# Performance work log

Measured on AMD Instinct MI355X. Metric: run time of the kernel, lower is better.

## Reference

```python
import jax, jax.numpy as jnp
import numpy as np

N = 50000   # nodes
E = 800000  # edges (avg degree 16)
D = 64      # isize == hidden_dim
L = 3       # num_gc_layers
BN_EPS = 1e-5


def setup_inputs() -> dict:
    key = jax.random.key(0)
    ks = jax.random.split(key, 8)
    x = jax.random.normal(ks[0], (N, D), dtype=jnp.float32)
    edge_index = jax.random.randint(ks[1], (2, E), 0, N, dtype=jnp.int64)
    # Stacked per-layer MLP params (layer 0 has isize==hidden_dim so shapes match)
    scale = 0.05
    W1 = jax.random.normal(ks[2], (L, D, D), dtype=jnp.float32) * scale
    b1 = jax.random.normal(ks[3], (L, D), dtype=jnp.float32) * scale
    W2 = jax.random.normal(ks[4], (L, D, D), dtype=jnp.float32) * scale
    b2 = jax.random.normal(ks[5], (L, D), dtype=jnp.float32) * scale
    gamma = jnp.ones((L, D), dtype=jnp.float32)
    beta = jnp.zeros((L, D), dtype=jnp.float32)
    return {"x": x, "edge_index": edge_index, "W1": W1, "b1": b1,
            "W2": W2, "b2": b2, "gamma": gamma, "beta": beta}


def reference(x, edge_index, W1, b1, W2, b2, gamma, beta):
    # GINConv (eps=0): h_i' = MLP(x_i + sum_{j->i} x_j), then BatchNorm1d
    # (training-mode batch statistics), ReLU on all but the last layer.
    # Dropout is identity (deterministic / eval).
    src = edge_index[0]
    dst = edge_index[1]
    h = x
    for i in range(L):
        agg = jax.ops.segment_sum(h[src], dst, num_segments=N)  # [N, D] scatter-add
        z = h + agg                                             # (1+eps)*x + agg, eps=0
        z = jnp.maximum(z @ W1[i] + b1[i], 0.0)                 # MLP hidden + ReLU
        z = z @ W2[i] + b2[i]                                   # MLP out
        mean = jnp.mean(z, axis=0)
        var = jnp.var(z, axis=0)                                # biased var, as torch BN
        z = (z - mean) * jax.lax.rsqrt(var + BN_EPS) * gamma[i] + beta[i]
        if i < L - 1:
            z = jnp.maximum(z, 0.0)
        h = z
    return h
```

## Files before the change

kernel.cpp:

```cpp
#include <hip/hip_runtime.h>

#define NN 50000
#define NPAD 50064
#define EE 800000
#define DD 64
#define BN_EPS 1e-5f

#define NPART 8
#define PART_NODES 6250
#define CAP 64
#define BCAP 131072
#define NSCAT 32
#define NB_BUCKET 782
#define NB_AGG  12500
#define NB_MLP  782
#define NB_SETUP 1563
#define NB_APPLY 3125

typedef __attribute__((ext_vector_type(8))) short short8v;
typedef __attribute__((ext_vector_type(4))) float float4v;

__device__ __forceinline__ unsigned bfpack2(float a, float b) {
    union { float f; unsigned u; } ua, ub;
    ua.f = a; ub.f = b;
    unsigned ra = ua.u + 0x7fffu + ((ua.u >> 16) & 1u);
    unsigned rb = ub.u + 0x7fffu + ((ub.u >> 16) & 1u);
    return (ra >> 16) | (rb & 0xffff0000u);
}

__device__ __forceinline__ unsigned short bf16of(float v) {
    union { float f; unsigned u; } x; x.f = v;
    unsigned r = x.u + 0x7fffu + ((x.u >> 16) & 1u);
    return (unsigned short)(r >> 16);
}

__global__ __launch_bounds__(256) void k_setup(const float* __restrict__ x,
                                               unsigned* __restrict__ xb,
                                               const float* __restrict__ W1,
                                               const float* __restrict__ W2,
                                               unsigned short* __restrict__ Wb,
                                               int* __restrict__ bucketCnt,
                                               float* __restrict__ stats) {
    int t = blockIdx.x * 256 + threadIdx.x;
    if (t < NN * 8) {
        const float4* p = (const float4*)(x + (size_t)t * 8);
        float4 a = p[0], b = p[1];
        uint4 o;
        o.x = bfpack2(a.x, a.y); o.y = bfpack2(a.z, a.w);
        o.z = bfpack2(b.x, b.y); o.w = bfpack2(b.z, b.w);
        ((uint4*)xb)[t] = o;
    }
    if (t < 3 * 2 * 4096) {
        int l = t / 8192;
        int rem = t - l * 8192;
        int m = rem / 4096;
        int e = rem - m * 4096;
        int c = e >> 6, k = e & 63;
        const float* W = (m == 0 ? W1 : W2) + l * 4096;
        Wb[t] = bf16of(W[k * 64 + c]);
    }
    if (t < 128) bucketCnt[t] = 0;
    else if (t < 512) stats[t - 128] = 0.f;
}

__global__ __launch_bounds__(1024) void k_build(const int* __restrict__ src,
                                                const int* __restrict__ dst,
                                                unsigned long long* __restrict__ bucket,
                                                int* __restrict__ bucketCnt,
                                                int* __restrict__ cursor) {
    __shared__ int lcnt[8];
    __shared__ int lbase[8];
    int t = threadIdx.x;
    int g = blockIdx.x * 1024 + t;
    if (g < NN) cursor[g] = 0;
    if (t < 8) lcnt[t] = 0;
    __syncthreads();
    int d = 0, s = 0, p = 0, loc = 0;
    bool ok = (g < EE);
    if (ok) {
        d = __builtin_nontemporal_load(dst + g);
        s = __builtin_nontemporal_load(src + g);
        p = (unsigned)d / PART_NODES;
        loc = atomicAdd(&lcnt[p], 1);
    }
    __syncthreads();
    if (t < 8) lbase[t] = atomicAdd(&bucketCnt[t * 16], lcnt[t]);
    __syncthreads();
    if (ok) {
        unsigned long long v = ((unsigned long long)(unsigned)s << 32) | (unsigned)d;
        bucket[(size_t)p * BCAP + lbase[p] + loc] = v;
    }
}

__global__ __launch_bounds__(256) void k_scatter(const unsigned long long* __restrict__ bucket,
                                                 const int* __restrict__ bucketCnt,
                                                 int* __restrict__ cursor,
                                                 int* __restrict__ col) {
    int p = blockIdx.x & 7;
    int cnt = bucketCnt[p * 16];
    const unsigned long long* b = bucket + (size_t)p * BCAP;
    for (int i = (blockIdx.x >> 3) * 256 + threadIdx.x; i < cnt; i += NSCAT * 256) {
        unsigned long long v = __builtin_nontemporal_load(b + i);
        int d = (int)(v & 0xffffffffu);
        int s = (int)(v >> 32);
        int pos = atomicAdd(&cursor[d], 1);
        col[d * CAP + pos] = s;
    }
}

template<int FUSE>
__global__ __launch_bounds__(256) void k_agg4(const unsigned* __restrict__ hb,
                                              const int* __restrict__ deg,
                                              const int* __restrict__ col,
                                              const float* __restrict__ statsL,
                                              const float* __restrict__ gammaL,
                                              const float* __restrict__ betaL,
                                              unsigned* __restrict__ outZb) {
    __shared__ float sa[64];
    __shared__ float sc[64];
    if (FUSE) {
        int tt = threadIdx.x;
        if (tt < 64) {
            float mean = statsL[tt] * (1.f / NN);
            float var = statsL[64 + tt] * (1.f / NN) - mean * mean;
            float a = gammaL[tt] * rsqrtf(var + BN_EPS);
            sa[tt] = a;
            sc[tt] = fmaf(-mean, a, betaL[tt]);
        }
        __syncthreads();
    }
    int node = blockIdx.x * 4 + (threadIdx.x >> 6);
    int lane = threadIdx.x & 63;
    int li = lane & 7;
    int slot = lane >> 3;
    int dn = deg[node];
    int base = node * CAP;
    const uint4* hb4 = (const uint4*)hb;
    float a8[8], c8[8];
    if (FUSE) {
#pragma unroll
        for (int j = 0; j < 8; ++j) { a8[j] = sa[li * 8 + j]; c8[j] = sc[li * 8 + j]; }
    }
    float acc[8];
#pragma unroll
    for (int i = 0; i < 8; ++i) acc[i] = 0.f;

#define UNPK_ADD(U)                                                      \
    {                                                                    \
        uint4 _u = (U);                                                  \
        union { unsigned u; float f; } l0, h0, l1, h1, l2, h2, l3, h3;   \
        l0.u = _u.x << 16; h0.u = _u.x & 0xffff0000u;                    \
        l1.u = _u.y << 16; h1.u = _u.y & 0xffff0000u;                    \
        l2.u = _u.z << 16; h2.u = _u.z & 0xffff0000u;                    \
        l3.u = _u.w << 16; h3.u = _u.w & 0xffff0000u;                    \
        float v[8] = {l0.f, h0.f, l1.f, h1.f, l2.f, h2.f, l3.f, h3.f};   \
        _Pragma("unroll")                                                \
        for (int j = 0; j < 8; ++j)                                      \
            acc[j] += FUSE ? fmaxf(fmaf(v[j], a8[j], c8[j]), 0.f) : v[j];\
    }

    if (slot == 0)
        UNPK_ADD(hb4[(size_t)node * 8 + li]);

    int k = slot;
    for (; k + 8 < dn; k += 16) {
        int s0 = __builtin_nontemporal_load(col + base + k);
        int s1 = __builtin_nontemporal_load(col + base + k + 8);
        uint4 u0 = hb4[(size_t)s0 * 8 + li];
        uint4 u1 = hb4[(size_t)s1 * 8 + li];
        UNPK_ADD(u0);
        UNPK_ADD(u1);
    }
    if (k < dn) {
        int s0 = __builtin_nontemporal_load(col + base + k);
        UNPK_ADD(hb4[(size_t)s0 * 8 + li]);
    }
#undef UNPK_ADD

#pragma unroll
    for (int i = 0; i < 8; ++i) acc[i] += __shfl_xor(acc[i], 8);
#pragma unroll
    for (int i = 0; i < 8; ++i) acc[i] += __shfl_xor(acc[i], 16);
#pragma unroll
    for (int i = 0; i < 8; ++i) acc[i] += __shfl_xor(acc[i], 32);

    if (slot == 0) {
        uint4 o;
        o.x = bfpack2(acc[0], acc[1]);
        o.y = bfpack2(acc[2], acc[3]);
        o.z = bfpack2(acc[4], acc[5]);
        o.w = bfpack2(acc[6], acc[7]);
        ((uint4*)outZb)[(size_t)node * 8 + li] = o;
    }
}

template<int OUTF32>
__global__ __launch_bounds__(256) void k_mlp_mfma(const unsigned short* __restrict__ Zb,
                                                  const unsigned short* __restrict__ WbL,
                                                  const float* __restrict__ b1,
                                                  const float* __restrict__ b2,
                                                  unsigned short* __restrict__ Mb,
                                                  float* __restrict__ Zf,
                                                  float* __restrict__ statsL) {
    __shared__ unsigned short sm[4][16 * 72];
    __shared__ float sred[2][4][64];
    int w = threadIdx.x >> 6;
    int lane = threadIdx.x & 63;
    int q = lane >> 4;
    int cl = lane & 15;
    int r0 = blockIdx.x * 64 + w * 16;

    short8v B1[4][2], B2[4][2];
#pragma unroll
    for (int t = 0; t < 4; ++t) {
#pragma unroll
        for (int h = 0; h < 2; ++h) {
            B1[t][h] = *(const short8v*)(WbL + ((t * 16 + cl) * 64 + h * 32 + q * 8));
            B2[t][h] = *(const short8v*)(WbL + 4096 + ((t * 16 + cl) * 64 + h * 32 + q * 8));
        }
    }

    const unsigned short* zr = Zb + (size_t)(r0 + cl) * 64;
    short8v a0 = *(const short8v*)(zr + q * 8);
    short8v a1 = *(const short8v*)(zr + 32 + q * 8);

    float4v acc1[4];
#pragma unroll
    for (int t = 0; t < 4; ++t) {
        float b = b1[t * 16 + cl];
        acc1[t] = (float4v){b, b, b, b};
        acc1[t] = __builtin_amdgcn_mfma_f32_16x16x32_bf16(a0, B1[t][0], acc1[t], 0, 0, 0);
        acc1[t] = __builtin_amdgcn_mfma_f32_16x16x32_bf16(a1, B1[t][1], acc1[t], 0, 0, 0);
    }

    unsigned short* s = sm[w];
#pragma unroll
    for (int t = 0; t < 4; ++t) {
#pragma unroll
        for (int r = 0; r < 4; ++r) {
            float v = fmaxf(acc1[t][r], 0.f);
            s[(q * 4 + r) * 72 + t * 16 + cl] = bf16of(v);
        }
    }

    short8v a2_0 = *(const short8v*)(s + cl * 72 + q * 8);
    short8v a2_1 = *(const short8v*)(s + cl * 72 + 32 + q * 8);

    float4v acc2[4];
#pragma unroll
    for (int t = 0; t < 4; ++t) {
        float b = b2[t * 16 + cl];
        acc2[t] = (float4v){b, b, b, b};
        acc2[t] = __builtin_amdgcn_mfma_f32_16x16x32_bf16(a2_0, B2[t][0], acc2[t], 0, 0, 0);
        acc2[t] = __builtin_amdgcn_mfma_f32_16x16x32_bf16(a2_1, B2[t][1], acc2[t], 0, 0, 0);
    }

    if (OUTF32) {
#pragma unroll
        for (int t = 0; t < 4; ++t) {
#pragma unroll
            for (int r = 0; r < 4; ++r) {
                int row = r0 + q * 4 + r;
                if (row < NN) Zf[(size_t)row * 64 + t * 16 + cl] = acc2[t][r];
            }
        }
    } else {
#pragma unroll
        for (int t = 0; t < 4; ++t) {
#pragma unroll
            for (int r = 0; r < 4; ++r) {
                s[(q * 4 + r) * 72 + t * 16 + cl] = bf16of(acc2[t][r]);
            }
        }
        short8v m0 = *(const short8v*)(s + cl * 72 + q * 8);
        short8v m1 = *(const short8v*)(s + cl * 72 + 32 + q * 8);
        int orow = r0 + cl;
        if (orow < NN) {
            *(short8v*)(Mb + (size_t)orow * 64 + q * 8) = m0;
            *(short8v*)(Mb + (size_t)orow * 64 + 32 + q * 8) = m1;
        }
    }

#pragma unroll
    for (int t = 0; t < 4; ++t) {
        float sv = 0.f, qv = 0.f;
#pragma unroll
        for (int r = 0; r < 4; ++r) {
            int row = r0 + q * 4 + r;
            float v = (row < NN) ? acc2[t][r] : 0.f;
            sv += v;
            qv = fmaf(v, v, qv);
        }
        sv += __shfl_xor(sv, 16); sv += __shfl_xor(sv, 32);
        qv += __shfl_xor(qv, 16); qv += __shfl_xor(qv, 32);
        if (lane < 16) {
            sred[0][w][t * 16 + cl] = sv;
            sred[1][w][t * 16 + cl] = qv;
        }
    }
    __syncthreads();
    int tt = threadIdx.x;
    if (tt < 128) {
        int which = tt >> 6, c = tt & 63;
        float tot = sred[which][0][c] + sred[which][1][c] +
                    sred[which][2][c] + sred[which][3][c];
        atomicAdd(&statsL[which * 64 + c], tot);
    }
}

__global__ __launch_bounds__(256) void k_apply_aff(const float* __restrict__ B,
                                                   const float* __restrict__ statsL,
                                                   const float* __restrict__ gammaL,
                                                   const float* __restrict__ betaL,
                                                   float* __restrict__ out) {
    __shared__ float sa[64];
    __shared__ float sc[64];
    int t = threadIdx.x;
    if (t < 64) {
        float mean = statsL[t] * (1.f / NN);
        float var = statsL[64 + t] * (1.f / NN) - mean * mean;
        float a = gammaL[t] * rsqrtf(var + BN_EPS);
        sa[t] = a;
        sc[t] = fmaf(-mean, a, betaL[t]);
    }
    __syncthreads();
    int i4 = blockIdx.x * 256 + t;
    if (i4 >= NN * 16) return;
    int cb = (i4 & 15) * 4;
    float4 v = ((const float4*)B)[i4];
    float4 o;
    o.x = fmaf(v.x, sa[cb + 0], sc[cb + 0]);
    o.y = fmaf(v.y, sa[cb + 1], sc[cb + 1]);
    o.z = fmaf(v.z, sa[cb + 2], sc[cb + 2]);
    o.w = fmaf(v.w, sa[cb + 3], sc[cb + 3]);
    ((float4*)out)[i4] = o;
}

extern "C" void kernel_launch(void* const* d_in, const int* in_sizes, int n_in,
                              void* d_out, int out_size, void* d_ws, size_t ws_size,
                              hipStream_t stream) {
    const float* x     = (const float*)d_in[0];
    const int*   ei    = (const int*)d_in[1];
    const float* W1    = (const float*)d_in[2];
    const float* b1    = (const float*)d_in[3];
    const float* W2    = (const float*)d_in[4];
    const float* b2    = (const float*)d_in[5];
    const float* gamma = (const float*)d_in[6];
    const float* beta  = (const float*)d_in[7];
    float* out = (float*)d_out;

    const int* src = ei;
    const int* dst = ei + EE;

    char* w = (char*)d_ws;
    unsigned*       Ab  = (unsigned*)w;       w += (size_t)NPAD * DD * 2;
    unsigned*       Mb  = (unsigned*)w;       w += (size_t)NPAD * DD * 2;
    unsigned*       Xb  = (unsigned*)w;       w += (size_t)NPAD * DD * 2;
    float*          Zf  = (float*)w;          w += (size_t)NN * DD * 4;
    int*            col = (int*)w;            w += (size_t)NN * CAP * 4;
    unsigned long long* bucket = (unsigned long long*)w;
    w += (size_t)NPART * BCAP * 8;
    int*            cursor    = (int*)w;      w += (size_t)NN * 4;
    int*            bucketCnt = (int*)w;      w += 128 * 4;
    float*          stats     = (float*)w;    w += 384 * 4;
    unsigned short* Wb        = (unsigned short*)w; w += 3 * 2 * 4096 * 2;

    k_setup<<<NB_SETUP, 256, 0, stream>>>(x, Xb, W1, W2, Wb, bucketCnt, stats);
    k_build<<<NB_BUCKET, 1024, 0, stream>>>(src, dst, bucket, bucketCnt, cursor);
    k_scatter<<<NPART * NSCAT, 256, 0, stream>>>(bucket, bucketCnt, cursor, col);

    k_agg4<0><<<NB_AGG, 256, 0, stream>>>(Xb, cursor, col, nullptr, nullptr, nullptr, Ab);
    k_mlp_mfma<0><<<NB_MLP, 256, 0, stream>>>((unsigned short*)Ab, Wb, b1, b2,
                                              (unsigned short*)Mb, nullptr, stats);

    k_agg4<1><<<NB_AGG, 256, 0, stream>>>(Mb, cursor, col, stats, gamma, beta, Ab);
    k_mlp_mfma<0><<<NB_MLP, 256, 0, stream>>>((unsigned short*)Ab, Wb + 8192, b1 + 64, b2 + 64,
                                              (unsigned short*)Mb, nullptr, stats + 128);

    k_agg4<1><<<NB_AGG, 256, 0, stream>>>(Mb, cursor, col, stats + 128, gamma + 64, beta + 64, Ab);
    k_mlp_mfma<1><<<NB_MLP, 256, 0, stream>>>((unsigned short*)Ab, Wb + 16384, b1 + 128, b2 + 128,
                                              nullptr, Zf, stats + 256);
    k_apply_aff<<<NB_APPLY, 256, 0, stream>>>(Zf, stats + 256, gamma + 128, beta + 128, out);
}
```

Before: 234.9 us.

## Fuse BatchNorm into MLP via grid barrier and compact edge buckets

The MLP kernel now accumulates the BatchNorm statistics, waits at a software grid-wide barrier (an atomic counter plus a spin-wait), and then applies the normalization and ReLU before writing bf16 output. This removes the fp32 intermediate buffer, the separate apply kernel and the per-edge BN work in the aggregation kernels. Setup work (bf16 conversion of x and the weights) is folded into the bucket-build kernel, and edge buckets are packed into 32-bit words instead of 64-bit. The spin barrier relies on all 782 blocks being resident at once (launch_bounds 256,4), so it can deadlock if occupancy is lower than assumed.

New measurement: 397.4 us. 69.2% more time.

```diff
diff --git a/kernel.cpp b/kernel.cpp
--- a/kernel.cpp
+++ b/kernel.cpp
@@ -11,11 +11,9 @@
 #define CAP 64
 #define BCAP 131072
 #define NSCAT 32
-#define NB_BUCKET 782
+#define NB_BUILD 782
 #define NB_AGG  12500
 #define NB_MLP  782
-#define NB_SETUP 1563
-#define NB_APPLY 3125
 
 typedef __attribute__((ext_vector_type(8))) short short8v;
 typedef __attribute__((ext_vector_type(4))) float float4v;
@@ -34,101 +32,85 @@
     return (unsigned short)(r >> 16);
 }
 
-__global__ __launch_bounds__(256) void k_setup(const float* __restrict__ x,
-                                               unsigned* __restrict__ xb,
-                                               const float* __restrict__ W1,
-                                               const float* __restrict__ W2,
-                                               unsigned short* __restrict__ Wb,
-                                               int* __restrict__ bucketCnt,
-                                               float* __restrict__ stats) {
-    int t = blockIdx.x * 256 + threadIdx.x;
-    if (t < NN * 8) {
-        const float4* p = (const float4*)(x + (size_t)t * 8);
-        float4 a = p[0], b = p[1];
-        uint4 o;
-        o.x = bfpack2(a.x, a.y); o.y = bfpack2(a.z, a.w);
-        o.z = bfpack2(b.x, b.y); o.w = bfpack2(b.z, b.w);
-        ((uint4*)xb)[t] = o;
-    }
-    if (t < 3 * 2 * 4096) {
-        int l = t / 8192;
-        int rem = t - l * 8192;
-        int m = rem / 4096;
-        int e = rem - m * 4096;
-        int c = e >> 6, k = e & 63;
-        const float* W = (m == 0 ? W1 : W2) + l * 4096;
-        Wb[t] = bf16of(W[k * 64 + c]);
-    }
+__global__ void k_zero(int* __restrict__ bucketCnt, float* __restrict__ stats) {
+    int t = threadIdx.x;
     if (t < 128) bucketCnt[t] = 0;
-    else if (t < 512) stats[t - 128] = 0.f;
+    if (t < 384) stats[t] = 0.f;
 }
 
 __global__ __launch_bounds__(1024) void k_build(const int* __restrict__ src,
                                                 const int* __restrict__ dst,
-                                                unsigned long long* __restrict__ bucket,
+                                                unsigned* __restrict__ bucket,
                                                 int* __restrict__ bucketCnt,
-                                                int* __restrict__ cursor) {
+                                                int* __restrict__ cursor,
+                                                const float* __restrict__ x,
+                                                unsigned* __restrict__ xb,
+                                                const float* __restrict__ W1,
+                                                const float* __restrict__ W2,
+                                                unsigned short* __restrict__ Wb) {
     __shared__ int lcnt[8];
     __shared__ int lbase[8];
     int t = threadIdx.x;
     int g = blockIdx.x * 1024 + t;
     if (g < NN) cursor[g] = 0;
+    if (g < NN * 8) {
+        const float4* p = (const float4*)(x + (size_t)g * 8);
+        float4 a = p[0], b = p[1];
+        uint4 o;
+        o.x = bfpack2(a.x, a.y); o.y = bfpack2(a.z, a.w);
+        o.z = bfpack2(b.x, b.y); o.w = bfpack2(b.z, b.w);
+        ((uint4*)xb)[g] = o;
+    }
+    if (g < 3 * 2 * 4096) {
+        int l = g / 8192;
+        int rem = g - l * 8192;
+        int m = rem / 4096;
+        int e = rem - m * 4096;
+        int c = e >> 6, k = e & 63;
+        const float* W = (m == 0 ? W1 : W2) + l * 4096;
+        Wb[g] = bf16of(W[k * 64 + c]);
+    }
     if (t < 8) lcnt[t] = 0;
     __syncthreads();
-    int d = 0, s = 0, p = 0, loc = 0;
+    int p = 0, loc = 0;
+    unsigned pk = 0;
     bool ok = (g < EE);
     if (ok) {
-        d = __builtin_nontemporal_load(dst + g);
-        s = __builtin_nontemporal_load(src + g);
+        int d = __builtin_nontemporal_load(dst + g);
+        int s = __builtin_nontemporal_load(src + g);
         p = (unsigned)d / PART_NODES;
+        pk = ((unsigned)s << 13) | (unsigned)(d - p * PART_NODES);
         loc = atomicAdd(&lcnt[p], 1);
     }
     __syncthreads();
     if (t < 8) lbase[t] = atomicAdd(&bucketCnt[t * 16], lcnt[t]);
     __syncthreads();
-    if (ok) {
-        unsigned long long v = ((unsigned long long)(unsigned)s << 32) | (unsigned)d;
-        bucket[(size_t)p * BCAP + lbase[p] + loc] = v;
-    }
-}
-
-__global__ __launch_bounds__(256) void k_scatter(const unsigned long long* __restrict__ bucket,
+    if (ok) bucket[(size_t)p * BCAP + lbase[p] + loc] = pk;
+}
+
+__global__ __launch_bounds__(256) void k_scatter(const unsigned* __restrict__ bucket,
                                                  const int* __restrict__ bucketCnt,
                                                  int* __restrict__ cursor,
                                                  int* __restrict__ col) {
     int p = blockIdx.x & 7;
     int cnt = bucketCnt[p * 16];
-    const unsigned long long* b = bucket + (size_t)p * BCAP;
+    int dbase = p * PART_NODES;
+    const unsigned* b = bucket + (size_t)p * BCAP;
     for (int i = (blockIdx.x >> 3) * 256 + threadIdx.x; i < cnt; i += NSCAT * 256) {
-        unsigned long long v = __builtin_nontemporal_load(b + i);
-        int d = (int)(v & 0xffffffffu);
-        int s = (int)(v >> 32);
+        unsigned v = __builtin_nontemporal_load(b + i);
+        int d = dbase + (int)(v & 8191u);
+        int s = (int)(v >> 13);
         int pos = atomicAdd(&cursor[d], 1);
         col[d * CAP + pos] = s;
     }
 }
 
-template<int FUSE>
 __global__ __launch_bounds__(256) void k_agg4(const unsigned* __restrict__ hb,
                                               const int* __restrict__ deg,
                                               const int* __restrict__ col,
-                                              const float* __restrict__ statsL,
-                                              const float* __restrict__ gammaL,
-                                              const float* __restrict__ betaL,
+                                              int* __restrict__ bcnt,
                                               unsigned* __restrict__ outZb) {
-    __shared__ float sa[64];
-    __shared__ float sc[64];
-    if (FUSE) {
-        int tt = threadIdx.x;
-        if (tt < 64) {
-            float mean = statsL[tt] * (1.f / NN);
-            float var = statsL[64 + tt] * (1.f / NN) - mean * mean;
-            float a = gammaL[tt] * rsqrtf(var + BN_EPS);
-            sa[tt] = a;
-            sc[tt] = fmaf(-mean, a, betaL[tt]);
-        }
-        __syncthreads();
-    }
+    if (blockIdx.x == 0 && threadIdx.x == 0) *bcnt = 0;
     int node = blockIdx.x * 4 + (threadIdx.x >> 6);
     int lane = threadIdx.x & 63;
     int li = lane & 7;
@@ -136,11 +118,6 @@
     int dn = deg[node];
     int base = node * CAP;
     const uint4* hb4 = (const uint4*)hb;
-    float a8[8], c8[8];
-    if (FUSE) {
-#pragma unroll
-        for (int j = 0; j < 8; ++j) { a8[j] = sa[li * 8 + j]; c8[j] = sc[li * 8 + j]; }
-    }
     float acc[8];
 #pragma unroll
     for (int i = 0; i < 8; ++i) acc[i] = 0.f;
@@ -153,10 +130,8 @@
         l1.u = _u.y << 16; h1.u = _u.y & 0xffff0000u;                    \
         l2.u = _u.z << 16; h2.u = _u.z & 0xffff0000u;                    \
         l3.u = _u.w << 16; h3.u = _u.w & 0xffff0000u;                    \
-        float v[8] = {l0.f, h0.f, l1.f, h1.f, l2.f, h2.f, l3.f, h3.f};   \
-        _Pragma("unroll")                                                \
-        for (int j = 0; j < 8; ++j)                                      \
-            acc[j] += FUSE ? fmaxf(fmaf(v[j], a8[j], c8[j]), 0.f) : v[j];\
+        acc[0] += l0.f; acc[1] += h0.f; acc[2] += l1.f; acc[3] += h1.f;  \
+        acc[4] += l2.f; acc[5] += h2.f; acc[6] += l3.f; acc[7] += h3.f;  \
     }
 
     if (slot == 0)
@@ -194,30 +169,33 @@
     }
 }
 
-template<int OUTF32>
-__global__ __launch_bounds__(256) void k_mlp_mfma(const unsigned short* __restrict__ Zb,
+template<int FINAL>
+__global__ __launch_bounds__(256, 4) void k_mlpbn(const unsigned short* __restrict__ Zb,
                                                   const unsigned short* __restrict__ WbL,
                                                   const float* __restrict__ b1,
                                                   const float* __restrict__ b2,
+                                                  const float* __restrict__ gammaL,
+                                                  const float* __restrict__ betaL,
+                                                  float* __restrict__ statsL,
+                                                  int* __restrict__ bcnt,
                                                   unsigned short* __restrict__ Mb,
-                                                  float* __restrict__ Zf,
-                                                  float* __restrict__ statsL) {
+                                                  float* __restrict__ outF) {
     __shared__ unsigned short sm[4][16 * 72];
     __shared__ float sred[2][4][64];
+    __shared__ float sa[64];
+    __shared__ float sc[64];
     int w = threadIdx.x >> 6;
     int lane = threadIdx.x & 63;
     int q = lane >> 4;
     int cl = lane & 15;
     int r0 = blockIdx.x * 64 + w * 16;
 
-    short8v B1[4][2], B2[4][2];
-#pragma unroll
-    for (int t = 0; t < 4; ++t) {
-#pragma unroll
-        for (int h = 0; h < 2; ++h) {
+    short8v B1[4][2];
+#pragma unroll
+    for (int t = 0; t < 4; ++t) {
+#pragma unroll
+        for (int h = 0; h < 2; ++h)
             B1[t][h] = *(const short8v*)(WbL + ((t * 16 + cl) * 64 + h * 32 + q * 8));
-            B2[t][h] = *(const short8v*)(WbL + 4096 + ((t * 16 + cl) * 64 + h * 32 + q * 8));
-        }
     }
 
     const unsigned short* zr = Zb + (size_t)(r0 + cl) * 64;
@@ -246,6 +224,14 @@
     short8v a2_0 = *(const short8v*)(s + cl * 72 + q * 8);
     short8v a2_1 = *(const short8v*)(s + cl * 72 + 32 + q * 8);
 
+    short8v B2[4][2];
+#pragma unroll
+    for (int t = 0; t < 4; ++t) {
+#pragma unroll
+        for (int h = 0; h < 2; ++h)
+            B2[t][h] = *(const short8v*)(WbL + 4096 + ((t * 16 + cl) * 64 + h * 32 + q * 8));
+    }
+
     float4v acc2[4];
 #pragma unroll
     for (int t = 0; t < 4; ++t) {
@@ -255,23 +241,71 @@
         acc2[t] = __builtin_amdgcn_mfma_f32_16x16x32_bf16(a2_1, B2[t][1], acc2[t], 0, 0, 0);
     }
 
-    if (OUTF32) {
+#pragma unroll
+    for (int t = 0; t < 4; ++t) {
+        float sv = 0.f, qv = 0.f;
+#pragma unroll
+        for (int r = 0; r < 4; ++r) {
+            int row = r0 + q * 4 + r;
+            float v = (row < NN) ? acc2[t][r] : 0.f;
+            sv += v;
+            qv = fmaf(v, v, qv);
+        }
+        sv += __shfl_xor(sv, 16); sv += __shfl_xor(sv, 32);
+        qv += __shfl_xor(qv, 16); qv += __shfl_xor(qv, 32);
+        if (lane < 16) {
+            sred[0][w][t * 16 + cl] = sv;
+            sred[1][w][t * 16 + cl] = qv;
+        }
+    }
+    __syncthreads();
+    int tt = threadIdx.x;
+    if (tt < 128) {
+        int which = tt >> 6, c = tt & 63;
+        float tot = sred[which][0][c] + sred[which][1][c] +
+                    sred[which][2][c] + sred[which][3][c];
+        atomicAdd(&statsL[which * 64 + c], tot);
+    }
+
+    __syncthreads();
+    if (tt == 0) {
+        __threadfence();
+        atomicAdd(bcnt, 1);
+        while (__hip_atomic_load(bcnt, __ATOMIC_ACQUIRE, __HIP_MEMORY_SCOPE_AGENT) < NB_MLP) {}
+    }
+    __syncthreads();
+
+    if (tt < 64) {
+        float mean = statsL[tt] * (1.f / NN);
+        float var = statsL[64 + tt] * (1.f / NN) - mean * mean;
+        float a = gammaL[tt] * rsqrtf(var + BN_EPS);
+        sa[tt] = a;
+        sc[tt] = fmaf(-mean, a, betaL[tt]);
+    }
+    __syncthreads();
+
+    if (FINAL) {
 #pragma unroll
         for (int t = 0; t < 4; ++t) {
+            float a = sa[t * 16 + cl], c = sc[t * 16 + cl];
 #pragma unroll
             for (int r = 0; r < 4; ++r) {
                 int row = r0 + q * 4 + r;
-                if (row < NN) Zf[(size_t)row * 64 + t * 16 + cl] = acc2[t][r];
+                if (row < NN)
+                    outF[(size_t)row * 64 + t * 16 + cl] = fmaf(acc2[t][r], a, c);
             }
         }
     } else {
 #pragma unroll
         for (int t = 0; t < 4; ++t) {
+            float a = sa[t * 16 + cl], c = sc[t * 16 + cl];
 #pragma unroll
             for (int r = 0; r < 4; ++r) {
-                s[(q * 4 + r) * 72 + t * 16 + cl] = bf16of(acc2[t][r]);
+                float y = fmaxf(fmaf(acc2[t][r], a, c), 0.f);
+                s[(q * 4 + r) * 72 + t * 16 + cl] = bf16of(y);
             }
         }
+        __syncthreads();
         short8v m0 = *(const short8v*)(s + cl * 72 + q * 8);
         short8v m1 = *(const short8v*)(s + cl * 72 + 32 + q * 8);
         int orow = r0 + cl;
@@ -280,60 +314,6 @@
             *(short8v*)(Mb + (size_t)orow * 64 + 32 + q * 8) = m1;
         }
     }
-
-#pragma unroll
-    for (int t = 0; t < 4; ++t) {
-        float sv = 0.f, qv = 0.f;
-#pragma unroll
-        for (int r = 0; r < 4; ++r) {
-            int row = r0 + q * 4 + r;
-            float v = (row < NN) ? acc2[t][r] : 0.f;
-            sv += v;
-            qv = fmaf(v, v, qv);
-        }
-        sv += __shfl_xor(sv, 16); sv += __shfl_xor(sv, 32);
-        qv += __shfl_xor(qv, 16); qv += __shfl_xor(qv, 32);
-        if (lane < 16) {
-            sred[0][w][t * 16 + cl] = sv;
-            sred[1][w][t * 16 + cl] = qv;
-        }
-    }
-    __syncthreads();
-    int tt = threadIdx.x;
-    if (tt < 128) {
-        int which = tt >> 6, c = tt & 63;
-        float tot = sred[which][0][c] + sred[which][1][c] +
-                    sred[which][2][c] + sred[which][3][c];
-        atomicAdd(&statsL[which * 64 + c], tot);
-    }
-}
-
-__global__ __launch_bounds__(256) void k_apply_aff(const float* __restrict__ B,
-                                                   const float* __restrict__ statsL,
-                                                   const float* __restrict__ gammaL,
-                                                   const float* __restrict__ betaL,
-                                                   float* __restrict__ out) {
-    __shared__ float sa[64];
-    __shared__ float sc[64];
-    int t = threadIdx.x;
-    if (t < 64) {
-        float mean = statsL[t] * (1.f / NN);
-        float var = statsL[64 + t] * (1.f / NN) - mean * mean;
-        float a = gammaL[t] * rsqrtf(var + BN_EPS);
-        sa[t] = a;
-        sc[t] = fmaf(-mean, a, betaL[t]);
-    }
-    __syncthreads();
-    int i4 = blockIdx.x * 256 + t;
-    if (i4 >= NN * 16) return;
-    int cb = (i4 & 15) * 4;
-    float4 v = ((const float4*)B)[i4];
-    float4 o;
-    o.x = fmaf(v.x, sa[cb + 0], sc[cb + 0]);
-    o.y = fmaf(v.y, sa[cb + 1], sc[cb + 1]);
-    o.z = fmaf(v.z, sa[cb + 2], sc[cb + 2]);
-    o.w = fmaf(v.w, sa[cb + 3], sc[cb + 3]);
-    ((float4*)out)[i4] = o;
 }
 
 extern "C" void kernel_launch(void* const* d_in, const int* in_sizes, int n_in,
@@ -356,29 +336,31 @@
     unsigned*       Ab  = (unsigned*)w;       w += (size_t)NPAD * DD * 2;
     unsigned*       Mb  = (unsigned*)w;       w += (size_t)NPAD * DD * 2;
     unsigned*       Xb  = (unsigned*)w;       w += (size_t)NPAD * DD * 2;
-    float*          Zf  = (float*)w;          w += (size_t)NN * DD * 4;
     int*            col = (int*)w;            w += (size_t)NN * CAP * 4;
-    unsigned long long* bucket = (unsigned long long*)w;
-    w += (size_t)NPART * BCAP * 8;
+    unsigned*       bucket = (unsigned*)w;    w += (size_t)NPART * BCAP * 4;
     int*            cursor    = (int*)w;      w += (size_t)NN * 4;
     int*            bucketCnt = (int*)w;      w += 128 * 4;
     float*          stats     = (float*)w;    w += 384 * 4;
+    int*            bcnt      = (int*)w;      w += 16 * 4;
     unsigned short* Wb        = (unsigned short*)w; w += 3 * 2 * 4096 * 2;
 
-    k_setup<<<NB_SETUP, 256, 0, stream>>>(x, Xb, W1, W2, Wb, bucketCnt, stats);
-    k_build<<<NB_BUCKET, 1024, 0, stream>>>(src, dst, bucket, bucketCnt, cursor);
+    k_zero<<<1, 512, 0, stream>>>(bucketCnt, stats);
+    k_build<<<NB_BUILD, 1024, 0, stream>>>(src, dst, bucket, bucketCnt, cursor,
+                                           x, Xb, W1, W2, Wb);
     k_scatter<<<NPART * NSCAT, 256, 0, stream>>>(bucket, bucketCnt, cursor, col);
 
-    k_agg4<0><<<NB_AGG, 256, 0, stream>>>(Xb, cursor, col, nullptr, nullptr, nullptr, Ab);
-    k_mlp_mfma<0><<<NB_MLP, 256, 0, stream>>>((unsigned short*)Ab, Wb, b1, b2,
-                                              (unsigned short*)Mb, nullptr, stats);
-
-    k_agg4<1><<<NB_AGG, 256, 0, stream>>>(Mb, cursor, col, stats, gamma, beta, Ab);
-    k_mlp_mfma<0><<<NB_MLP, 256, 0, stream>>>((unsigned short*)Ab, Wb + 8192, b1 + 64, b2 + 64,
-                                              (unsigned short*)Mb, nullptr, stats + 128);
-
-    k_agg4<1><<<NB_AGG, 256, 0, stream>>>(Mb, cursor, col, stats + 128, gamma + 64, beta + 64, Ab);
-    k_mlp_mfma<1><<<NB_MLP, 256, 0, stream>>>((unsigned short*)Ab, Wb + 16384, b1 + 128, b2 + 128,
-                                              nullptr, Zf, stats + 256);
-    k_apply_aff<<<NB_APPLY, 256, 0, stream>>>(Zf, stats + 256, gamma + 128, beta + 128, out);
-}
+    k_agg4<<<NB_AGG, 256, 0, stream>>>(Xb, cursor, col, bcnt, Ab);
+    k_mlpbn<0><<<NB_MLP, 256, 0, stream>>>((unsigned short*)Ab, Wb, b1, b2,
+                                           gamma, beta, stats, bcnt,
+                                           (unsigned short*)Mb, nullptr);
+
+    k_agg4<<<NB_AGG, 256, 0, stream>>>(Mb, cursor, col, bcnt + 4, Ab);
+    k_mlpbn<0><<<NB_MLP, 256, 0, stream>>>((unsigned short*)Ab, Wb + 8192, b1 + 64, b2 + 64,
+                                           gamma + 64, beta + 64, stats + 128, bcnt + 4,
+                                           (unsigned short*)Mb, nullptr);
+
+    k_agg4<<<NB_AGG, 256, 0, stream>>>(Mb, cursor, col, bcnt + 8, Ab);
+    k_mlpbn<1><<<NB_MLP, 256, 0, stream>>>((unsigned short*)Ab, Wb + 16384, b1 + 128, b2 + 128,
+                                           gamma + 128, beta + 128, stats + 256, bcnt + 8,
+                                           nullptr, out);
+}
```

## Fuse setup into bucket build, pack bucket entries to 32 bits, widen agg lanes

Applied to the files above, without the earlier changes.

The x and weight bf16 conversion moves into the edge bucketing kernel, and only a tiny zeroing kernel stays separate, so one launch carries both jobs. Bucket entries shrink from 64-bit to 32-bit by storing the source plus a 13-bit destination offset within its partition, halving bucket write and read traffic. The aggregation kernel now uses 4 lanes per row with two uint4 loads each, letting 16 edges be gathered in parallel per node with one edge per slot per iteration. The trade-offs are more registers per lane and a longer shuffle reduction.

Result: slower. 280.3 us (+19.3%).

```diff
diff --git a/kernel.cpp b/kernel.cpp
--- a/kernel.cpp
+++ b/kernel.cpp
@@ -11,10 +11,9 @@
 #define CAP 64
 #define BCAP 131072
 #define NSCAT 32
-#define NB_BUCKET 782
+#define NB_BUILD 782
 #define NB_AGG  12500
 #define NB_MLP  782
-#define NB_SETUP 1563
 #define NB_APPLY 3125
 
 typedef __attribute__((ext_vector_type(8))) short short8v;
@@ -34,82 +33,81 @@
     return (unsigned short)(r >> 16);
 }
 
-__global__ __launch_bounds__(256) void k_setup(const float* __restrict__ x,
-                                               unsigned* __restrict__ xb,
-                                               const float* __restrict__ W1,
-                                               const float* __restrict__ W2,
-                                               unsigned short* __restrict__ Wb,
-                                               int* __restrict__ bucketCnt,
-                                               float* __restrict__ stats) {
-    int t = blockIdx.x * 256 + threadIdx.x;
-    if (t < NN * 8) {
-        const float4* p = (const float4*)(x + (size_t)t * 8);
-        float4 a = p[0], b = p[1];
-        uint4 o;
-        o.x = bfpack2(a.x, a.y); o.y = bfpack2(a.z, a.w);
-        o.z = bfpack2(b.x, b.y); o.w = bfpack2(b.z, b.w);
-        ((uint4*)xb)[t] = o;
-    }
-    if (t < 3 * 2 * 4096) {
-        int l = t / 8192;
-        int rem = t - l * 8192;
-        int m = rem / 4096;
-        int e = rem - m * 4096;
-        int c = e >> 6, k = e & 63;
-        const float* W = (m == 0 ? W1 : W2) + l * 4096;
-        Wb[t] = bf16of(W[k * 64 + c]);
-    }
+__global__ void k_zero(int* __restrict__ bucketCnt, float* __restrict__ stats) {
+    int t = threadIdx.x;
     if (t < 128) bucketCnt[t] = 0;
-    else if (t < 512) stats[t - 128] = 0.f;
+    if (t < 384) stats[t] = 0.f;
 }
 
 __global__ __launch_bounds__(1024) void k_build(const int* __restrict__ src,
                                                 const int* __restrict__ dst,
-                                                unsigned long long* __restrict__ bucket,
+                                                unsigned* __restrict__ bucket,
                                                 int* __restrict__ bucketCnt,
-                                                int* __restrict__ cursor) {
+                                                int* __restrict__ cursor,
+                                                const float* __restrict__ x,
+                                                unsigned* __restrict__ xb,
+                                                const float* __restrict__ W1,
+                                                const float* __restrict__ W2,
+                                                unsigned short* __restrict__ Wb) {
     __shared__ int lcnt[8];
     __shared__ int lbase[8];
     int t = threadIdx.x;
     int g = blockIdx.x * 1024 + t;
     if (g < NN) cursor[g] = 0;
+    if (g < NN * 8) {
+        const float4* p = (const float4*)(x + (size_t)g * 8);
+        float4 a = p[0], b = p[1];
+        uint4 o;
+        o.x = bfpack2(a.x, a.y); o.y = bfpack2(a.z, a.w);
+        o.z = bfpack2(b.x, b.y); o.w = bfpack2(b.z, b.w);
+        ((uint4*)xb)[g] = o;
+    }
+    if (g < 3 * 2 * 4096) {
+        int l = g / 8192;
+        int rem = g - l * 8192;
+        int m = rem / 4096;
+        int e = rem - m * 4096;
+        int c = e >> 6, k = e & 63;
+        const float* W = (m == 0 ? W1 : W2) + l * 4096;
+        Wb[g] = bf16of(W[k * 64 + c]);
+    }
     if (t < 8) lcnt[t] = 0;
     __syncthreads();
-    int d = 0, s = 0, p = 0, loc = 0;
+    int p = 0, loc = 0;
+    unsigned pk = 0;
     bool ok = (g < EE);
     if (ok) {
-        d = __builtin_nontemporal_load(dst + g);
-        s = __builtin_nontemporal_load(src + g);
+        int d = __builtin_nontemporal_load(dst + g);
+        int s = __builtin_nontemporal_load(src + g);
         p = (unsigned)d / PART_NODES;
+        pk = ((unsigned)s << 13) | (unsigned)(d - p * PART_NODES);
         loc = atomicAdd(&lcnt[p], 1);
     }
     __syncthreads();
     if (t < 8) lbase[t] = atomicAdd(&bucketCnt[t * 16], lcnt[t]);
     __syncthreads();
-    if (ok) {
-        unsigned long long v = ((unsigned long long)(unsigned)s << 32) | (unsigned)d;
-        bucket[(size_t)p * BCAP + lbase[p] + loc] = v;
-    }
-}
-
-__global__ __launch_bounds__(256) void k_scatter(const unsigned long long* __restrict__ bucket,
+    if (ok) bucket[(size_t)p * BCAP + lbase[p] + loc] = pk;
+}
+
+__global__ __launch_bounds__(256) void k_scatter(const unsigned* __restrict__ bucket,
                                                  const int* __restrict__ bucketCnt,
                                                  int* __restrict__ cursor,
                                                  int* __restrict__ col) {
     int p = blockIdx.x & 7;
     int cnt = bucketCnt[p * 16];
-    const unsigned long long* b = bucket + (size_t)p * BCAP;
+    int dbase = p * PART_NODES;
+    const unsigned* b = bucket + (size_t)p * BCAP;
     for (int i = (blockIdx.x >> 3) * 256 + threadIdx.x; i < cnt; i += NSCAT * 256) {
-        unsigned long long v = __builtin_nontemporal_load(b + i);
-        int d = (int)(v & 0xffffffffu);
-        int s = (int)(v >> 32);
+        unsigned v = __builtin_nontemporal_load(b + i);
+        int d = dbase + (int)(v & 8191u);
+        int s = (int)(v >> 13);
         int pos = atomicAdd(&cursor[d], 1);
         col[d * CAP + pos] = s;
     }
 }
 
 template<int FUSE>
-__global__ __launch_bounds__(256) void k_agg4(const unsigned* __restrict__ hb,
+__global__ __launch_bounds__(256) void k_agg5(const unsigned* __restrict__ hb,
                                               const int* __restrict__ deg,
                                               const int* __restrict__ col,
                                               const float* __restrict__ statsL,
@@ -131,66 +129,71 @@
     }
     int node = blockIdx.x * 4 + (threadIdx.x >> 6);
     int lane = threadIdx.x & 63;
-    int li = lane & 7;
-    int slot = lane >> 3;
+    int li = lane & 3;
+    int slot = lane >> 2;
     int dn = deg[node];
     int base = node * CAP;
     const uint4* hb4 = (const uint4*)hb;
-    float a8[8], c8[8];
+    float a16[16], c16[16];
     if (FUSE) {
 #pragma unroll
-        for (int j = 0; j < 8; ++j) { a8[j] = sa[li * 8 + j]; c8[j] = sc[li * 8 + j]; }
-    }
-    float acc[8];
-#pragma unroll
-    for (int i = 0; i < 8; ++i) acc[i] = 0.f;
-
-#define UNPK_ADD(U)                                                      \
-    {                                                                    \
-        uint4 _u = (U);                                                  \
-        union { unsigned u; float f; } l0, h0, l1, h1, l2, h2, l3, h3;   \
-        l0.u = _u.x << 16; h0.u = _u.x & 0xffff0000u;                    \
-        l1.u = _u.y << 16; h1.u = _u.y & 0xffff0000u;                    \
-        l2.u = _u.z << 16; h2.u = _u.z & 0xffff0000u;                    \
-        l3.u = _u.w << 16; h3.u = _u.w & 0xffff0000u;                    \
-        float v[8] = {l0.f, h0.f, l1.f, h1.f, l2.f, h2.f, l3.f, h3.f};   \
-        _Pragma("unroll")                                                \
-        for (int j = 0; j < 8; ++j)                                      \
-            acc[j] += FUSE ? fmaxf(fmaf(v[j], a8[j], c8[j]), 0.f) : v[j];\
-    }
-
-    if (slot == 0)
-        UNPK_ADD(hb4[(size_t)node * 8 + li]);
-
-    int k = slot;
-    for (; k + 8 < dn; k += 16) {
-        int s0 = __builtin_nontemporal_load(col + base + k);
-        int s1 = __builtin_nontemporal_load(col + base + k + 8);
-        uint4 u0 = hb4[(size_t)s0 * 8 + li];
-        uint4 u1 = hb4[(size_t)s1 * 8 + li];
-        UNPK_ADD(u0);
-        UNPK_ADD(u1);
-    }
-    if (k < dn) {
-        int s0 = __builtin_nontemporal_load(col + base + k);
-        UNPK_ADD(hb4[(size_t)s0 * 8 + li]);
-    }
-#undef UNPK_ADD
-
-#pragma unroll
-    for (int i = 0; i < 8; ++i) acc[i] += __shfl_xor(acc[i], 8);
-#pragma unroll
-    for (int i = 0; i < 8; ++i) acc[i] += __shfl_xor(acc[i], 16);
-#pragma unroll
-    for (int i = 0; i < 8; ++i) acc[i] += __shfl_xor(acc[i], 32);
+        for (int j = 0; j < 8; ++j) {
+            a16[j] = sa[li * 8 + j];      c16[j] = sc[li * 8 + j];
+            a16[8 + j] = sa[32 + li * 8 + j]; c16[8 + j] = sc[32 + li * 8 + j];
+        }
+    }
+    float acc[16];
+#pragma unroll
+    for (int i = 0; i < 16; ++i) acc[i] = 0.f;
+
+#define UNPK_ADD2(U0, U1)                                                 \
+    {                                                                     \
+        uint4 _a = (U0), _b = (U1);                                       \
+        unsigned uu[8] = {_a.x, _a.y, _a.z, _a.w, _b.x, _b.y, _b.z, _b.w};\
+        _Pragma("unroll")                                                 \
+        for (int j = 0; j < 8; ++j) {                                     \
+            union { unsigned u; float f; } lo, hi;                        \
+            lo.u = uu[j] << 16; hi.u = uu[j] & 0xffff0000u;               \
+            int e0 = (j < 4) ? 2 * j : 8 + 2 * (j - 4);                   \
+            float v0 = lo.f, v1 = hi.f;                                   \
+            if (FUSE) {                                                   \
+                v0 = fmaxf(fmaf(v0, a16[e0], c16[e0]), 0.f);              \
+                v1 = fmaxf(fmaf(v1, a16[e0 + 1], c16[e0 + 1]), 0.f);      \
+            }                                                             \
+            acc[e0] += v0; acc[e0 + 1] += v1;                             \
+        }                                                                 \
+    }
 
     if (slot == 0) {
-        uint4 o;
-        o.x = bfpack2(acc[0], acc[1]);
-        o.y = bfpack2(acc[2], acc[3]);
-        o.z = bfpack2(acc[4], acc[5]);
-        o.w = bfpack2(acc[6], acc[7]);
-        ((uint4*)outZb)[(size_t)node * 8 + li] = o;
+        uint4 s0 = hb4[(size_t)node * 8 + li];
+        uint4 s1 = hb4[(size_t)node * 8 + 4 + li];
+        UNPK_ADD2(s0, s1);
+    }
+
+    for (int k = slot; k < dn; k += 16) {
+        int s = __builtin_nontemporal_load(col + base + k);
+        uint4 u0 = hb4[(size_t)s * 8 + li];
+        uint4 u1 = hb4[(size_t)s * 8 + 4 + li];
+        UNPK_ADD2(u0, u1);
+    }
+#undef UNPK_ADD2
+
+#pragma unroll
+    for (int i = 0; i < 16; ++i) {
+        acc[i] += __shfl_xor(acc[i], 4);
+        acc[i] += __shfl_xor(acc[i], 8);
+        acc[i] += __shfl_xor(acc[i], 16);
+        acc[i] += __shfl_xor(acc[i], 32);
+    }
+
+    if (slot == 0) {
+        uint4 o0, o1;
+        o0.x = bfpack2(acc[0], acc[1]);   o0.y = bfpack2(acc[2], acc[3]);
+        o0.z = bfpack2(acc[4], acc[5]);   o0.w = bfpack2(acc[6], acc[7]);
+        o1.x = bfpack2(acc[8], acc[9]);   o1.y = bfpack2(acc[10], acc[11]);
+        o1.z = bfpack2(acc[12], acc[13]); o1.w = bfpack2(acc[14], acc[15]);
+        ((uint4*)outZb)[(size_t)node * 8 + li] = o0;
+        ((uint4*)outZb)[(size_t)node * 8 + 4 + li] = o1;
     }
 }
 
@@ -358,26 +361,26 @@
     unsigned*       Xb  = (unsigned*)w;       w += (size_t)NPAD * DD * 2;
     float*          Zf  = (float*)w;          w += (size_t)NN * DD * 4;
     int*            col = (int*)w;            w += (size_t)NN * CAP * 4;
-    unsigned long long* bucket = (unsigned long long*)w;
-    w += (size_t)NPART * BCAP * 8;
+    unsigned*       bucket = (unsigned*)w;    w += (size_t)NPART * BCAP * 4;
     int*            cursor    = (int*)w;      w += (size_t)NN * 4;
     int*            bucketCnt = (int*)w;      w += 128 * 4;
     float*          stats     = (float*)w;    w += 384 * 4;
     unsigned short* Wb        = (unsigned short*)w; w += 3 * 2 * 4096 * 2;
 
-    k_setup<<<NB_SETUP, 256, 0, stream>>>(x, Xb, W1, W2, Wb, bucketCnt, stats);
-    k_build<<<NB_BUCKET, 1024, 0, stream>>>(src, dst, bucket, bucketCnt, cursor);
+    k_zero<<<1, 512, 0, stream>>>(bucketCnt, stats);
+    k_build<<<NB_BUILD, 1024, 0, stream>>>(src, dst, bucket, bucketCnt, cursor,
+                                           x, Xb, W1, W2, Wb);
     k_scatter<<<NPART * NSCAT, 256, 0, stream>>>(bucket, bucketCnt, cursor, col);
 
-    k_agg4<0><<<NB_AGG, 256, 0, stream>>>(Xb, cursor, col, nullptr, nullptr, nullptr, Ab);
+    k_agg5<0><<<NB_AGG, 256, 0, stream>>>(Xb, cursor, col, nullptr, nullptr, nullptr, Ab);
     k_mlp_mfma<0><<<NB_MLP, 256, 0, stream>>>((unsigned short*)Ab, Wb, b1, b2,
                                               (unsigned short*)Mb, nullptr, stats);
 
-    k_agg4<1><<<NB_AGG, 256, 0, stream>>>(Mb, cursor, col, stats, gamma, beta, Ab);
+    k_agg5<1><<<NB_AGG, 256, 0, stream>>>(Mb, cursor, col, stats, gamma, beta, Ab);
     k_mlp_mfma<0><<<NB_MLP, 256, 0, stream>>>((unsigned short*)Ab, Wb + 8192, b1 + 64, b2 + 64,
                                               (unsigned short*)Mb, nullptr, stats + 128);
 
-    k_agg4<1><<<NB_AGG, 256, 0, stream>>>(Mb, cursor, col, stats + 128, gamma + 64, beta + 64, Ab);
+    k_agg5<1><<<NB_AGG, 256, 0, stream>>>(Mb, cursor, col, stats + 128, gamma + 64, beta + 64, Ab);
     k_mlp_mfma<1><<<NB_MLP, 256, 0, stream>>>((unsigned short*)Ab, Wb + 16384, b1 + 128, b2 + 128,
                                               nullptr, Zf, stats + 256);
     k_apply_aff<<<NB_APPLY, 256, 0, stream>>>(Zf, stats + 256, gamma + 128, beta + 128, out);
```
